# Optimization experiments

Hardware: AMD Instinct MI355X
Metric: run time of the kernel (lower is better)

The kernel has to match this reference:

```python
import jax, jax.numpy as jnp
import numpy as np

D_MODEL, NHEAD, INT_DIM = 1024, 16, 4096
HEAD_DIM = D_MODEL // NHEAD
EPS = 1e-5


def _layernorm(x, gamma, beta):
    mu = jnp.mean(x, axis=-1, keepdims=True)
    var = jnp.var(x, axis=-1, keepdims=True)
    return (x - mu) * jax.lax.rsqrt(var + EPS) * gamma + beta


def setup_inputs() -> dict:
    key = jax.random.key(0)
    ks = jax.random.split(key, 16)
    B, T = 2, 2048
    s = 0.02
    inp = {
        'x': jax.random.normal(ks[0], (B, T, D_MODEL), dtype=jnp.float32),
        'Wq': jax.random.normal(ks[1], (D_MODEL, D_MODEL), dtype=jnp.float32) * s,
        'bq': jnp.zeros((D_MODEL,), jnp.float32),
        'Wk': jax.random.normal(ks[2], (D_MODEL, D_MODEL), dtype=jnp.float32) * s,
        'bk': jnp.zeros((D_MODEL,), jnp.float32),
        'Wv': jax.random.normal(ks[3], (D_MODEL, D_MODEL), dtype=jnp.float32) * s,
        'bv': jnp.zeros((D_MODEL,), jnp.float32),
        'Wo': jax.random.normal(ks[4], (D_MODEL, D_MODEL), dtype=jnp.float32) * s,
        'bo': jnp.zeros((D_MODEL,), jnp.float32),
        'ln1_g': jnp.ones((D_MODEL,), jnp.float32),
        'ln1_b': jnp.zeros((D_MODEL,), jnp.float32),
        'ln2_g': jnp.ones((D_MODEL,), jnp.float32),
        'ln2_b': jnp.zeros((D_MODEL,), jnp.float32),
        'W1': jax.random.normal(ks[5], (D_MODEL, INT_DIM), dtype=jnp.float32) * s,
        'b1': jnp.zeros((INT_DIM,), jnp.float32),
        'W2': jax.random.normal(ks[6], (INT_DIM, D_MODEL), dtype=jnp.float32) * s,
        'b2': jnp.zeros((D_MODEL,), jnp.float32),
    }
    return inp


def reference(x, Wq, bq, Wk, bk, Wv, bv, Wo, bo, ln1_g, ln1_b, ln2_g, ln2_b, W1, b1, W2, b2):
    B, T, D = x.shape
    # projections
    q = (x @ Wq + bq).reshape(B, T, NHEAD, HEAD_DIM).transpose(0, 2, 1, 3)
    k = (x @ Wk + bk).reshape(B, T, NHEAD, HEAD_DIM).transpose(0, 2, 1, 3)
    v = (x @ Wv + bv).reshape(B, T, NHEAD, HEAD_DIM).transpose(0, 2, 1, 3)
    # attention: [B,H,T,T] scores, softmax over keys
    scores = jnp.einsum('bhqd,bhkd->bhqk', q, k) / jnp.sqrt(jnp.float32(HEAD_DIM))
    attn = jax.nn.softmax(scores, axis=-1)
    out = jnp.einsum('bhqk,bhkd->bhqd', attn, v)
    out = out.transpose(0, 2, 1, 3).reshape(B, T, D)
    attn_output = out @ Wo + bo
    # residual + layernorm 1
    h = _layernorm(x + attn_output, ln1_g, ln1_b)
    # FFN
    ff = jax.nn.relu(h @ W1 + b1) @ W2 + b2
    # residual + layernorm 2
    return _layernorm(h + ff, ln2_g, ln2_b)
```

## Files before the change

kernel.cpp:

```cpp
#include <hip/hip_runtime.h>
#include <cstdint>

#define DEVI __device__ __forceinline__

typedef float f32x4 __attribute__((ext_vector_type(4)));
typedef __bf16 bf16x8 __attribute__((ext_vector_type(8)));
typedef unsigned short u16;
typedef unsigned int u32;
typedef unsigned long long u64;

DEVI u16 bf16bits(float f) {
    u32 u = __builtin_bit_cast(u32, f);
    u32 r = u + 0x7fffu + ((u >> 16) & 1u);
    return (u16)(r >> 16);
}

DEVI u32 pack2bf(float a, float b) {
    u16 x = __builtin_bit_cast(u16, (__bf16)a);
    u16 y = __builtin_bit_cast(u16, (__bf16)b);
    return (u32)x | ((u32)y << 16);
}

DEVI void gload16(const void* g, const void* l) {
    __builtin_amdgcn_global_load_lds(
        (const __attribute__((address_space(1))) void*)(u64)(uintptr_t)g,
        (__attribute__((address_space(3))) void*)(u32)(uintptr_t)l,
        16, 0, 0);
}

__global__ __launch_bounds__(256) void cast_bf16_kernel(const float* __restrict__ in,
                                                        u16* __restrict__ out, int n4) {
    int i = blockIdx.x * 256 + threadIdx.x;
    if (i < n4) {
        float4 v = ((const float4*)in)[i];
        u32 lo = bf16bits(v.x) | ((u32)bf16bits(v.y) << 16);
        u32 hi = bf16bits(v.z) | ((u32)bf16bits(v.w) << 16);
        ((uint2*)out)[i] = make_uint2(lo, hi);
    }
}

DEVI void tpose_body(const float* __restrict__ src, u16* __restrict__ dst, int K_, int N_) {
    __shared__ float t[64][65];
    int k0 = blockIdx.x * 64, n0 = blockIdx.y * 64;
    int tid = threadIdx.x;
#pragma unroll
    for (int i = 0; i < 16; i++) {
        int idx = i * 256 + tid;
        int r = idx >> 6, c = idx & 63;
        t[r][c] = src[(u64)(k0 + r) * N_ + n0 + c];
    }
    __syncthreads();
#pragma unroll
    for (int i = 0; i < 16; i++) {
        int idx = i * 256 + tid;
        int r = idx >> 6, c = idx & 63;
        dst[(u64)(n0 + r) * K_ + k0 + c] = bf16bits(t[c][r]);
    }
}

__global__ __launch_bounds__(256) void transpose_cast_kernel(const float* __restrict__ src,
                                                             u16* __restrict__ dst,
                                                             int K_, int N_) {
    tpose_body(src, dst, K_, N_);
}

__global__ __launch_bounds__(256) void transpose_cast4_kernel(
    const float* __restrict__ s0, const float* __restrict__ s1,
    const float* __restrict__ s2, const float* __restrict__ s3,
    u16* __restrict__ d0, u16* __restrict__ d1, u16* __restrict__ d2, u16* __restrict__ d3) {
    int z = blockIdx.z;
    const float* src = z == 0 ? s0 : z == 1 ? s1 : z == 2 ? s2 : s3;
    u16* dst = z == 0 ? d0 : z == 1 ? d1 : z == 2 ? d2 : d3;
    tpose_body(src, dst, 1024, 1024);
}

enum { MODE_QK = 0, MODE_VT = 1, MODE_RESID = 2, MODE_RELU = 3 };

DEVI void gemm_core(const u16* __restrict__ A, const u16* __restrict__ Bt, int K_,
                    u16* ldsA, u16* ldsB, f32x4 (&acc)[4][4], int m0, int n0) {
    const int tid = threadIdx.x;
    const int lane = tid & 63;
    const int wid = tid >> 6;
    const int wr = wid >> 1, wc = wid & 1;
    const int l15 = lane & 15, l4 = lane >> 4;

    for (int kt = 0; kt < K_; kt += 64) {
        __syncthreads();
#pragma unroll
        for (int i = 0; i < 4; i++) {
            int s = i * 256 + tid;
            int row = s >> 3, c = s & 7;
            gload16(A + (u64)(m0 + row) * K_ + kt + ((c ^ (row & 7)) * 8),
                    (const char*)ldsA + s * 16);
        }
#pragma unroll
        for (int i = 0; i < 4; i++) {
            int s = i * 256 + tid;
            int row = s >> 3, c = s & 7;
            gload16(Bt + (u64)(n0 + row) * K_ + kt + ((c ^ (row & 7)) * 8),
                    (const char*)ldsB + s * 16);
        }
        __syncthreads();
#pragma unroll
        for (int ks = 0; ks < 2; ks++) {
            bf16x8 af[4], bfr[4];
#pragma unroll
            for (int mi = 0; mi < 4; mi++) {
                int row = wr * 64 + mi * 16 + l15;
                af[mi] = *(const bf16x8*)((const char*)ldsA + row * 128 +
                                          (((ks * 4 + l4) ^ (row & 7)) * 16));
            }
#pragma unroll
            for (int ni = 0; ni < 4; ni++) {
                int row = wc * 64 + ni * 16 + l15;
                bfr[ni] = *(const bf16x8*)((const char*)ldsB + row * 128 +
                                           (((ks * 4 + l4) ^ (row & 7)) * 16));
            }
            __builtin_amdgcn_s_setprio(1);
#pragma unroll
            for (int mi = 0; mi < 4; mi++)
#pragma unroll
                for (int ni = 0; ni < 4; ni++)
                    acc[mi][ni] = __builtin_amdgcn_mfma_f32_16x16x32_bf16(
                        af[mi], bfr[ni], acc[mi][ni], 0, 0, 0);
            __builtin_amdgcn_s_setprio(0);
        }
    }
}

template <int MODE>
DEVI void gemm_epilogue(f32x4 (&acc)[4][4], const float* __restrict__ bias,
                        const float* __restrict__ resid, void* __restrict__ outp,
                        int N_, int m0, int n0) {
    const int tid = threadIdx.x;
    const int lane = tid & 63;
    const int wid = tid >> 6;
    const int wr = wid >> 1, wc = wid & 1;
    const int l15 = lane & 15, l4 = lane >> 4;
#pragma unroll
    for (int mi = 0; mi < 4; mi++) {
#pragma unroll
        for (int ni = 0; ni < 4; ni++) {
            const int n = n0 + wc * 64 + ni * 16 + l15;
            const float bv = bias[n];
            const int mb = m0 + wr * 64 + mi * 16 + l4 * 4;
            if (MODE == MODE_VT) {
                const int b = mb >> 11, t = mb & 2047;
                const int hh = n >> 6, d = n & 63;
                u32 lo = pack2bf(acc[mi][ni][0] + bv, acc[mi][ni][1] + bv);
                u32 hi = pack2bf(acc[mi][ni][2] + bv, acc[mi][ni][3] + bv);
                u64 idx = ((u64)((b << 4) + hh) * 64 + d) * 2048 + t;
                *(uint2*)((u16*)outp + idx) = make_uint2(lo, hi);
            } else {
#pragma unroll
                for (int r = 0; r < 4; r++) {
                    const int m = mb + r;
                    const float v = acc[mi][ni][r] + bv;
                    if (MODE == MODE_QK) {
                        const int b = m >> 11, t = m & 2047;
                        const int hh = n >> 6, d = n & 63;
                        ((u16*)outp)[(((u64)((b << 4) + hh) * 2048 + t) << 6) + d] = bf16bits(v);
                    } else if (MODE == MODE_RESID) {
                        const u64 i2 = (u64)m * N_ + n;
                        ((float*)outp)[i2] = v + resid[i2];
                    } else {
                        ((u16*)outp)[(u64)m * N_ + n] = bf16bits(fmaxf(v, 0.f));
                    }
                }
            }
        }
    }
}

template <int MODE>
__global__ __launch_bounds__(256, 2)
void gemm_kernel(const u16* __restrict__ A, const u16* __restrict__ Bt,
                 const float* __restrict__ bias, const float* __restrict__ resid,
                 void* __restrict__ outp, int N_, int K_) {
    __shared__ u16 ldsA[128 * 64];
    __shared__ u16 ldsB[128 * 64];
    const int m0 = blockIdx.x * 128;
    const int n0 = blockIdx.y * 128;
    f32x4 acc[4][4];
#pragma unroll
    for (int i = 0; i < 4; i++)
#pragma unroll
        for (int j = 0; j < 4; j++) acc[i][j] = (f32x4){0.f, 0.f, 0.f, 0.f};
    gemm_core(A, Bt, K_, ldsA, ldsB, acc, m0, n0);
    gemm_epilogue<MODE>(acc, bias, resid, outp, N_, m0, n0);
}

__global__ __launch_bounds__(256, 2)
void gemm_qkv_kernel(const u16* __restrict__ A,
                     const u16* __restrict__ Wq, const u16* __restrict__ Wk,
                     const u16* __restrict__ Wv,
                     const float* __restrict__ bq, const float* __restrict__ bk,
                     const float* __restrict__ bv,
                     u16* __restrict__ Qo, u16* __restrict__ Ko, u16* __restrict__ Vo) {
    __shared__ u16 ldsA[128 * 64];
    __shared__ u16 ldsB[128 * 64];
    const int z = blockIdx.z;
    const u16* Bt = z == 0 ? Wq : z == 1 ? Wk : Wv;
    const float* bias = z == 0 ? bq : z == 1 ? bk : bv;
    const int m0 = blockIdx.x * 128;
    const int n0 = blockIdx.y * 128;
    f32x4 acc[4][4];
#pragma unroll
    for (int i = 0; i < 4; i++)
#pragma unroll
        for (int j = 0; j < 4; j++) acc[i][j] = (f32x4){0.f, 0.f, 0.f, 0.f};
    gemm_core(A, Bt, 1024, ldsA, ldsB, acc, m0, n0);
    if (z == 2)
        gemm_epilogue<MODE_VT>(acc, bias, nullptr, Vo, 1024, m0, n0);
    else
        gemm_epilogue<MODE_QK>(acc, bias, nullptr, z == 0 ? Qo : Ko, 1024, m0, n0);
}

#define LOG2E 1.44269504088896f

__global__ __launch_bounds__(256, 4)
void attn_kernel(const u16* __restrict__ Qg, const u16* __restrict__ Kg,
                 const u16* __restrict__ Vtg, u16* __restrict__ Og) {
    __shared__ u16 ldsK[2][64 * 64];
    __shared__ u16 ldsV[2][64 * 64];
    __shared__ u16 ldsP[4][16 * 64];
    const int tid = threadIdx.x;
    const int lane = tid & 63;
    const int w = tid >> 6;
    const int l15 = lane & 15, l4 = lane >> 4;
    const int id = blockIdx.x;
    const int swz = (id & 7) * 128 + (id >> 3);
    const int bh = swz >> 5;
    const int qblk = swz & 31;
    const u64 kvbase = (u64)bh * 2048 * 64;
    const int qw0 = qblk * 64 + w * 16;

    auto stage = [&](int buf, int kt) {
#pragma unroll
        for (int i = 0; i < 2; i++) {
            int s = i * 256 + tid; int row = s >> 3, c = s & 7;
            gload16(Kg + kvbase + (u64)(kt + row) * 64 + ((c ^ (row & 7)) * 8),
                    (const char*)ldsK[buf] + s * 16);
        }
#pragma unroll
        for (int i = 0; i < 2; i++) {
            int s = i * 256 + tid; int row = s >> 3, c = s & 7;
            gload16(Vtg + kvbase + (u64)row * 2048 + kt + ((c ^ (row & 7)) * 8),
                    (const char*)ldsV[buf] + s * 16);
        }
    };

    stage(0, 0);

    bf16x8 aq[2];
#pragma unroll
    for (int ks = 0; ks < 2; ks++)
        aq[ks] = *(const bf16x8*)(Qg + kvbase + (u64)(qw0 + l15) * 64 + ks * 32 + l4 * 8);

    f32x4 acco[4];
#pragma unroll
    for (int i = 0; i < 4; i++) acco[i] = (f32x4){0.f, 0.f, 0.f, 0.f};
    float lacc = 0.f;

    u16* ldsPw = ldsP[w];
    const float sc = 0.125f * LOG2E;

    asm volatile("s_waitcnt vmcnt(0)" ::: "memory");
    __builtin_amdgcn_s_barrier();

    for (int t = 0; t < 32; t++) {
        const int cur = t & 1;
        if (t < 31) stage(cur ^ 1, (t + 1) * 64);
        const u16* K_ = ldsK[cur];
        const u16* V_ = ldsV[cur];

        f32x4 sf[4];
#pragma unroll
        for (int f = 0; f < 4; f++) sf[f] = (f32x4){0.f, 0.f, 0.f, 0.f};
#pragma unroll
        for (int ks = 0; ks < 2; ks++) {
            bf16x8 ak[4];
#pragma unroll
            for (int f = 0; f < 4; f++) {
                int row = f * 16 + l15;
                ak[f] = *(const bf16x8*)((const char*)K_ + row * 128 +
                                         (((ks * 4 + l4) ^ (row & 7)) * 16));
            }
            __builtin_amdgcn_s_setprio(1);
#pragma unroll
            for (int f = 0; f < 4; f++)
                sf[f] = __builtin_amdgcn_mfma_f32_16x16x32_bf16(ak[f], aq[ks], sf[f], 0, 0, 0);
            __builtin_amdgcn_s_setprio(0);
        }

#pragma unroll
        for (int f = 0; f < 4; f++) {
            float p0 = exp2f(sf[f][0] * sc);
            float p1 = exp2f(sf[f][1] * sc);
            float p2 = exp2f(sf[f][2] * sc);
            float p3 = exp2f(sf[f][3] * sc);
            lacc += (p0 + p1) + (p2 + p3);
            *(uint2*)((char*)ldsPw + l15 * 128 +
                      (((f * 2 + (l4 >> 1)) ^ (l15 & 7)) * 16) + (l4 & 1) * 8) =
                make_uint2(pack2bf(p0, p1), pack2bf(p2, p3));
        }

#pragma unroll
        for (int ks = 0; ks < 2; ks++) {
            bf16x8 pfrag = *(const bf16x8*)((const char*)ldsPw + l15 * 128 +
                                            (((ks * 4 + l4) ^ (l15 & 7)) * 16));
#pragma unroll
            for (int nf = 0; nf < 4; nf++) {
                int row = nf * 16 + l15;
                bf16x8 av = *(const bf16x8*)((const char*)V_ + row * 128 +
                                             (((ks * 4 + l4) ^ (row & 7)) * 16));
                __builtin_amdgcn_s_setprio(1);
                acco[nf] = __builtin_amdgcn_mfma_f32_16x16x32_bf16(av, pfrag, acco[nf], 0, 0, 0);
                __builtin_amdgcn_s_setprio(0);
            }
        }

        asm volatile("s_waitcnt vmcnt(0)" ::: "memory");
        __builtin_amdgcn_s_barrier();
    }

    lacc += __shfl_xor(lacc, 16, 64);
    lacc += __shfl_xor(lacc, 32, 64);
    const float inv = 1.f / lacc;

    const int b = bh >> 4, h = bh & 15;
    const int tq = qw0 + l15;
#pragma unroll
    for (int nf = 0; nf < 4; nf++) {
        const int d = nf * 16 + l4 * 4;
        u32 lo = pack2bf(acco[nf][0] * inv, acco[nf][1] * inv);
        u32 hi = pack2bf(acco[nf][2] * inv, acco[nf][3] * inv);
        *(uint2*)(Og + ((u64)(b * 2048 + tq) << 10) + h * 64 + d) = make_uint2(lo, hi);
    }
}

template <bool WB16>
__global__ __launch_bounds__(256, 4)
void ln_kernel(const float* __restrict__ in, const float* __restrict__ gam,
               const float* __restrict__ bet, float* __restrict__ outf,
               u16* __restrict__ outb) {
    __shared__ float red[2][4];
    const int row = blockIdx.x;
    const int tid = threadIdx.x;
    float4 v = ((const float4*)(in + (u64)row * 1024))[tid];
    float s = v.x + v.y + v.z + v.w;
    float sq = v.x * v.x + v.y * v.y + v.z * v.z + v.w * v.w;
#pragma unroll
    for (int sh = 1; sh < 64; sh <<= 1) {
        s += __shfl_xor(s, sh, 64);
        sq += __shfl_xor(sq, sh, 64);
    }
    if ((tid & 63) == 0) { red[0][tid >> 6] = s; red[1][tid >> 6] = sq; }
    __syncthreads();
    s = red[0][0] + red[0][1] + red[0][2] + red[0][3];
    sq = red[1][0] + red[1][1] + red[1][2] + red[1][3];
    float mu = s * (1.f / 1024.f);
    float var = sq * (1.f / 1024.f) - mu * mu;
    float inv = rsqrtf(var + 1e-5f);
    float4 g = ((const float4*)gam)[tid];
    float4 bb = ((const float4*)bet)[tid];
    float4 o;
    o.x = (v.x - mu) * inv * g.x + bb.x;
    o.y = (v.y - mu) * inv * g.y + bb.y;
    o.z = (v.z - mu) * inv * g.z + bb.z;
    o.w = (v.w - mu) * inv * g.w + bb.w;
    ((float4*)(outf + (u64)row * 1024))[tid] = o;
    if (WB16) {
        u32 lo = pack2bf(o.x, o.y);
        u32 hi = pack2bf(o.z, o.w);
        ((uint2*)(outb + (u64)row * 1024))[tid] = make_uint2(lo, hi);
    }
}

extern "C" void kernel_launch(void* const* d_in, const int* in_sizes, int n_in,
                              void* d_out, int out_size, void* d_ws, size_t ws_size,
                              hipStream_t stream) {
    (void)in_sizes; (void)n_in; (void)out_size; (void)ws_size;
    const float* x  = (const float*)d_in[0];
    const float* Wq = (const float*)d_in[1];
    const float* bq = (const float*)d_in[2];
    const float* Wk = (const float*)d_in[3];
    const float* bk = (const float*)d_in[4];
    const float* Wv = (const float*)d_in[5];
    const float* bv = (const float*)d_in[6];
    const float* Wo = (const float*)d_in[7];
    const float* bo = (const float*)d_in[8];
    const float* g1 = (const float*)d_in[9];
    const float* be1 = (const float*)d_in[10];
    const float* g2 = (const float*)d_in[11];
    const float* be2 = (const float*)d_in[12];
    const float* W1 = (const float*)d_in[13];
    const float* b1 = (const float*)d_in[14];
    const float* W2 = (const float*)d_in[15];
    const float* b2 = (const float*)d_in[16];

    char* ws = (char*)d_ws;
    const u64 MB = 1024ull * 1024ull;
    u16* xb    = (u16*)(ws + 0);
    u16* Wqt   = (u16*)(ws + 8 * MB);
    u16* Wkt   = (u16*)(ws + 10 * MB);
    u16* Wvt   = (u16*)(ws + 12 * MB);
    u16* Wot   = (u16*)(ws + 14 * MB);
    u16* W1t   = (u16*)(ws + 16 * MB);
    u16* W2t   = (u16*)(ws + 24 * MB);
    u16* Qb    = (u16*)(ws + 32 * MB);
    u16* Kb    = (u16*)(ws + 40 * MB);
    u16* Vtb   = (u16*)(ws + 48 * MB);
    u16* Ob    = (u16*)(ws + 56 * MB);
    float* pre1 = (float*)(ws + 64 * MB);
    float* hf  = (float*)(ws + 80 * MB);
    u16* hb    = (u16*)(ws + 96 * MB);
    u16* ffb   = (u16*)(ws + 104 * MB);
    float* pre2 = (float*)(ws + 64 * MB);

    cast_bf16_kernel<<<4096, 256, 0, stream>>>(x, xb, 1024 * 1024);
    transpose_cast4_kernel<<<dim3(16, 16, 4), 256, 0, stream>>>(Wq, Wk, Wv, Wo,
                                                                Wqt, Wkt, Wvt, Wot);
    transpose_cast_kernel<<<dim3(16, 64), 256, 0, stream>>>(W1, W1t, 1024, 4096);
    transpose_cast_kernel<<<dim3(64, 16), 256, 0, stream>>>(W2, W2t, 4096, 1024);

    gemm_qkv_kernel<<<dim3(32, 8, 3), 256, 0, stream>>>(xb, Wqt, Wkt, Wvt,
                                                        bq, bk, bv, Qb, Kb, Vtb);

    attn_kernel<<<1024, 256, 0, stream>>>(Qb, Kb, Vtb, Ob);

    gemm_kernel<MODE_RESID><<<dim3(32, 8), 256, 0, stream>>>(Ob, Wot, bo, x, pre1, 1024, 1024);
    ln_kernel<true><<<4096, 256, 0, stream>>>(pre1, g1, be1, hf, hb);
    gemm_kernel<MODE_RELU><<<dim3(32, 32), 256, 0, stream>>>(hb, W1t, b1, nullptr, ffb, 4096, 1024);
    gemm_kernel<MODE_RESID><<<dim3(32, 8), 256, 0, stream>>>(ffb, W2t, b2, hf, pre2, 1024, 4096);
    ln_kernel<false><<<4096, 256, 0, stream>>>(pre2, g2, be2, (float*)d_out, nullptr);
}
```

Baseline: 252.0 us.

## Rewrite attention with 32x32 MFMA, register-resident P via permlane swap, folded Q scale

The attention kernel moves from 16x16x32 to 32x32x16 bf16 MFMA, with 2 waves per block each owning 32 query rows. The softmax probabilities now stay in registers and are rearranged with v_permlane32_swap into the B-operand layout, which removes the LDS round trip for P. The 1/sqrt(d)*log2e scale is folded into the Q projection epilogue so the inner exp2 loop drops a multiply. Risks are higher register pressure, fewer threads per block to stage K/V tiles, and lower occupancy from launch_bounds(128,2).

```diff
diff --git a/kernel.cpp b/kernel.cpp
--- a/kernel.cpp
+++ b/kernel.cpp
@@ -4,10 +4,15 @@
 #define DEVI __device__ __forceinline__
 
 typedef float f32x4 __attribute__((ext_vector_type(4)));
+typedef float f32x16 __attribute__((ext_vector_type(16)));
 typedef __bf16 bf16x8 __attribute__((ext_vector_type(8)));
+typedef unsigned int u32x4v __attribute__((ext_vector_type(4)));
 typedef unsigned short u16;
 typedef unsigned int u32;
 typedef unsigned long long u64;
+
+#define LOG2E 1.44269504088896f
+#define QSCALE (0.125f * LOG2E)
 
 DEVI u16 bf16bits(float f) {
     u32 u = __builtin_bit_cast(u32, f);
@@ -131,7 +136,7 @@
 template <int MODE>
 DEVI void gemm_epilogue(f32x4 (&acc)[4][4], const float* __restrict__ bias,
                         const float* __restrict__ resid, void* __restrict__ outp,
-                        int N_, int m0, int n0) {
+                        int N_, int m0, int n0, float scale) {
     const int tid = threadIdx.x;
     const int lane = tid & 63;
     const int wid = tid >> 6;
@@ -159,7 +164,8 @@
                     if (MODE == MODE_QK) {
                         const int b = m >> 11, t = m & 2047;
                         const int hh = n >> 6, d = n & 63;
-                        ((u16*)outp)[(((u64)((b << 4) + hh) * 2048 + t) << 6) + d] = bf16bits(v);
+                        ((u16*)outp)[(((u64)((b << 4) + hh) * 2048 + t) << 6) + d] =
+                            bf16bits(v * scale);
                     } else if (MODE == MODE_RESID) {
                         const u64 i2 = (u64)m * N_ + n;
                         ((float*)outp)[i2] = v + resid[i2];
@@ -187,7 +193,7 @@
 #pragma unroll
         for (int j = 0; j < 4; j++) acc[i][j] = (f32x4){0.f, 0.f, 0.f, 0.f};
     gemm_core(A, Bt, K_, ldsA, ldsB, acc, m0, n0);
-    gemm_epilogue<MODE>(acc, bias, resid, outp, N_, m0, n0);
+    gemm_epilogue<MODE>(acc, bias, resid, outp, N_, m0, n0, 1.f);
 }
 
 __global__ __launch_bounds__(256, 2)
@@ -211,40 +217,38 @@
         for (int j = 0; j < 4; j++) acc[i][j] = (f32x4){0.f, 0.f, 0.f, 0.f};
     gemm_core(A, Bt, 1024, ldsA, ldsB, acc, m0, n0);
     if (z == 2)
-        gemm_epilogue<MODE_VT>(acc, bias, nullptr, Vo, 1024, m0, n0);
+        gemm_epilogue<MODE_VT>(acc, bias, nullptr, Vo, 1024, m0, n0, 1.f);
     else
-        gemm_epilogue<MODE_QK>(acc, bias, nullptr, z == 0 ? Qo : Ko, 1024, m0, n0);
-}
-
-#define LOG2E 1.44269504088896f
-
-__global__ __launch_bounds__(256, 4)
+        gemm_epilogue<MODE_QK>(acc, bias, nullptr, z == 0 ? Qo : Ko, 1024, m0, n0,
+                               z == 0 ? QSCALE : 1.f);
+}
+
+__global__ __launch_bounds__(128, 2)
 void attn_kernel(const u16* __restrict__ Qg, const u16* __restrict__ Kg,
                  const u16* __restrict__ Vtg, u16* __restrict__ Og) {
     __shared__ u16 ldsK[2][64 * 64];
     __shared__ u16 ldsV[2][64 * 64];
-    __shared__ u16 ldsP[4][16 * 64];
     const int tid = threadIdx.x;
     const int lane = tid & 63;
     const int w = tid >> 6;
-    const int l15 = lane & 15, l4 = lane >> 4;
+    const int l31 = lane & 31, l5 = lane >> 5;
     const int id = blockIdx.x;
     const int swz = (id & 7) * 128 + (id >> 3);
     const int bh = swz >> 5;
     const int qblk = swz & 31;
     const u64 kvbase = (u64)bh * 2048 * 64;
-    const int qw0 = qblk * 64 + w * 16;
+    const int qw0 = qblk * 64 + w * 32;
 
     auto stage = [&](int buf, int kt) {
 #pragma unroll
-        for (int i = 0; i < 2; i++) {
-            int s = i * 256 + tid; int row = s >> 3, c = s & 7;
+        for (int i = 0; i < 4; i++) {
+            int s = i * 128 + tid; int row = s >> 3, c = s & 7;
             gload16(Kg + kvbase + (u64)(kt + row) * 64 + ((c ^ (row & 7)) * 8),
                     (const char*)ldsK[buf] + s * 16);
         }
 #pragma unroll
-        for (int i = 0; i < 2; i++) {
-            int s = i * 256 + tid; int row = s >> 3, c = s & 7;
+        for (int i = 0; i < 4; i++) {
+            int s = i * 128 + tid; int row = s >> 3, c = s & 7;
             gload16(Vtg + kvbase + (u64)row * 2048 + kt + ((c ^ (row & 7)) * 8),
                     (const char*)ldsV[buf] + s * 16);
         }
@@ -252,18 +256,14 @@
 
     stage(0, 0);
 
-    bf16x8 aq[2];
-#pragma unroll
-    for (int ks = 0; ks < 2; ks++)
-        aq[ks] = *(const bf16x8*)(Qg + kvbase + (u64)(qw0 + l15) * 64 + ks * 32 + l4 * 8);
-
-    f32x4 acco[4];
-#pragma unroll
-    for (int i = 0; i < 4; i++) acco[i] = (f32x4){0.f, 0.f, 0.f, 0.f};
-    float lacc = 0.f;
-
-    u16* ldsPw = ldsP[w];
-    const float sc = 0.125f * LOG2E;
+    bf16x8 aq[4];
+#pragma unroll
+    for (int dc = 0; dc < 4; dc++)
+        aq[dc] = *(const bf16x8*)(Qg + kvbase + (u64)(qw0 + l31) * 64 + dc * 16 + l5 * 8);
+
+    f32x16 acco[2] = {};
+    float la0 = 0.f, la1 = 0.f, la2 = 0.f, la3 = 0.f;
+    const f32x16 fz = {};
 
     asm volatile("s_waitcnt vmcnt(0)" ::: "memory");
     __builtin_amdgcn_s_barrier();
@@ -274,48 +274,56 @@
         const u16* K_ = ldsK[cur];
         const u16* V_ = ldsV[cur];
 
-        f32x4 sf[4];
-#pragma unroll
-        for (int f = 0; f < 4; f++) sf[f] = (f32x4){0.f, 0.f, 0.f, 0.f};
-#pragma unroll
-        for (int ks = 0; ks < 2; ks++) {
+        f32x16 sf[2];
+#pragma unroll
+        for (int f = 0; f < 2; f++) {
+            const int row = f * 32 + l31;
             bf16x8 ak[4];
 #pragma unroll
-            for (int f = 0; f < 4; f++) {
-                int row = f * 16 + l15;
-                ak[f] = *(const bf16x8*)((const char*)K_ + row * 128 +
-                                         (((ks * 4 + l4) ^ (row & 7)) * 16));
+            for (int dc = 0; dc < 4; dc++)
+                ak[dc] = *(const bf16x8*)((const char*)K_ + row * 128 +
+                                          (((dc * 2 + l5) ^ (row & 7)) * 16));
+            __builtin_amdgcn_s_setprio(1);
+            sf[f] = __builtin_amdgcn_mfma_f32_32x32x16_bf16(ak[0], aq[0], fz, 0, 0, 0);
+#pragma unroll
+            for (int dc = 1; dc < 4; dc++)
+                sf[f] = __builtin_amdgcn_mfma_f32_32x32x16_bf16(ak[dc], aq[dc], sf[f], 0, 0, 0);
+            __builtin_amdgcn_s_setprio(0);
+        }
+
+#pragma unroll
+        for (int f = 0; f < 2; f++) {
+#pragma unroll
+            for (int k = 0; k < 16; k += 4) {
+                float p0 = exp2f(sf[f][k + 0]);
+                float p1 = exp2f(sf[f][k + 1]);
+                float p2 = exp2f(sf[f][k + 2]);
+                float p3 = exp2f(sf[f][k + 3]);
+                sf[f][k + 0] = p0; sf[f][k + 1] = p1;
+                sf[f][k + 2] = p2; sf[f][k + 3] = p3;
+                la0 += p0; la1 += p1; la2 += p2; la3 += p3;
             }
-            __builtin_amdgcn_s_setprio(1);
-#pragma unroll
-            for (int f = 0; f < 4; f++)
-                sf[f] = __builtin_amdgcn_mfma_f32_16x16x32_bf16(ak[f], aq[ks], sf[f], 0, 0, 0);
-            __builtin_amdgcn_s_setprio(0);
-        }
-
-#pragma unroll
-        for (int f = 0; f < 4; f++) {
-            float p0 = exp2f(sf[f][0] * sc);
-            float p1 = exp2f(sf[f][1] * sc);
-            float p2 = exp2f(sf[f][2] * sc);
-            float p3 = exp2f(sf[f][3] * sc);
-            lacc += (p0 + p1) + (p2 + p3);
-            *(uint2*)((char*)ldsPw + l15 * 128 +
-                      (((f * 2 + (l4 >> 1)) ^ (l15 & 7)) * 16) + (l4 & 1) * 8) =
-                make_uint2(pack2bf(p0, p1), pack2bf(p2, p3));
-        }
-
-#pragma unroll
-        for (int ks = 0; ks < 2; ks++) {
-            bf16x8 pfrag = *(const bf16x8*)((const char*)ldsPw + l15 * 128 +
-                                            (((ks * 4 + l4) ^ (l15 & 7)) * 16));
-#pragma unroll
-            for (int nf = 0; nf < 4; nf++) {
-                int row = nf * 16 + l15;
+        }
+
+#pragma unroll
+        for (int c = 0; c < 4; c++) {
+            const int F = c >> 1;
+            const int rb = 8 * (c & 1);
+            u32 w0 = pack2bf(sf[F][rb + 0], sf[F][rb + 1]);
+            u32 w1 = pack2bf(sf[F][rb + 2], sf[F][rb + 3]);
+            u32 w2 = pack2bf(sf[F][rb + 4], sf[F][rb + 5]);
+            u32 w3 = pack2bf(sf[F][rb + 6], sf[F][rb + 7]);
+            asm volatile("v_permlane32_swap_b32 %0, %1" : "+v"(w0), "+v"(w2));
+            asm volatile("v_permlane32_swap_b32 %0, %1" : "+v"(w1), "+v"(w3));
+            u32x4v pw = {w0, w1, w2, w3};
+            bf16x8 pb = __builtin_bit_cast(bf16x8, pw);
+#pragma unroll
+            for (int db = 0; db < 2; db++) {
+                const int row = db * 32 + l31;
                 bf16x8 av = *(const bf16x8*)((const char*)V_ + row * 128 +
-                                             (((ks * 4 + l4) ^ (row & 7)) * 16));
+                                             (((c * 2 + l5) ^ (row & 7)) * 16));
                 __builtin_amdgcn_s_setprio(1);
-                acco[nf] = __builtin_amdgcn_mfma_f32_16x16x32_bf16(av, pfrag, acco[nf], 0, 0, 0);
+                acco[db] = __builtin_amdgcn_mfma_f32_32x32x16_bf16(av, pb, acco[db], 0, 0, 0);
                 __builtin_amdgcn_s_setprio(0);
             }
         }
@@ -324,19 +332,21 @@
         __builtin_amdgcn_s_barrier();
     }
 
-    lacc += __shfl_xor(lacc, 16, 64);
+    float lacc = (la0 + la1) + (la2 + la3);
     lacc += __shfl_xor(lacc, 32, 64);
     const float inv = 1.f / lacc;
 
     const int b = bh >> 4, h = bh & 15;
-    const int tq = qw0 + l15;
-#pragma unroll
-    for (int nf = 0; nf < 4; nf++) {
-        const int d = nf * 16 + l4 * 4;
-        u32 lo = pack2bf(acco[nf][0] * inv, acco[nf][1] * inv);
-        u32 hi = pack2bf(acco[nf][2] * inv, acco[nf][3] * inv);
-        *(uint2*)(Og + ((u64)(b * 2048 + tq) << 10) + h * 64 + d) = make_uint2(lo, hi);
-    }
+    const int tq = qw0 + l31;
+#pragma unroll
+    for (int db = 0; db < 2; db++)
+#pragma unroll
+        for (int rq = 0; rq < 4; rq++) {
+            const int d = 32 * db + 8 * rq + 4 * l5;
+            u32 lo = pack2bf(acco[db][4 * rq + 0] * inv, acco[db][4 * rq + 1] * inv);
+            u32 hi = pack2bf(acco[db][4 * rq + 2] * inv, acco[db][4 * rq + 3] * inv);
+            *(uint2*)(Og + ((u64)(b * 2048 + tq) << 10) + h * 64 + d) = make_uint2(lo, hi);
+        }
 }
 
 template <bool WB16>
@@ -427,7 +437,7 @@
     gemm_qkv_kernel<<<dim3(32, 8, 3), 256, 0, stream>>>(xb, Wqt, Wkt, Wvt,
                                                         bq, bk, bv, Qb, Kb, Vtb);
 
-    attn_kernel<<<1024, 256, 0, stream>>>(Qb, Kb, Vtb, Ob);
+    attn_kernel<<<1024, 128, 0, stream>>>(Qb, Kb, Vtb, Ob);
 
     gemm_kernel<MODE_RESID><<<dim3(32, 8), 256, 0, stream>>>(Ob, Wot, bo, x, pre1, 1024, 1024);
     ln_kernel<true><<<4096, 256, 0, stream>>>(pre1, g1, be1, hf, hb);
```

Measured after the change: 259.7 us. 1.03x slower.

## Fold softmax scale into Q projection and shuffle P in registers via permlane swaps

Applied to the files above, without the earlier changes.

The softmax scale (1/sqrt(d)·log2e) is now applied to Q in the QKV GEMM epilogue, so the attention loop drops a multiply per score. The P tile is no longer written to and read back from per-wave LDS. Lanes exchange the packed bf16 probabilities with v_permlane32/16_swap so they arrive in MFMA B-operand layout. The V fragment loads are batched ahead of the MFMAs, and launch bounds rise to 5 blocks per CU since LDS use drops. This relies on the permlane lane mapping matching the fragment layout, and Q rounded to bf16 after scaling changes numerics slightly.

```diff
diff --git a/kernel.cpp b/kernel.cpp
--- a/kernel.cpp
+++ b/kernel.cpp
@@ -5,9 +5,13 @@
 
 typedef float f32x4 __attribute__((ext_vector_type(4)));
 typedef __bf16 bf16x8 __attribute__((ext_vector_type(8)));
+typedef unsigned int u32x4v __attribute__((ext_vector_type(4)));
 typedef unsigned short u16;
 typedef unsigned int u32;
 typedef unsigned long long u64;
+
+#define LOG2E 1.44269504088896f
+#define QSCALE (0.125f * LOG2E)
 
 DEVI u16 bf16bits(float f) {
     u32 u = __builtin_bit_cast(u32, f);
@@ -131,7 +135,7 @@
 template <int MODE>
 DEVI void gemm_epilogue(f32x4 (&acc)[4][4], const float* __restrict__ bias,
                         const float* __restrict__ resid, void* __restrict__ outp,
-                        int N_, int m0, int n0) {
+                        int N_, int m0, int n0, float scale) {
     const int tid = threadIdx.x;
     const int lane = tid & 63;
     const int wid = tid >> 6;
@@ -159,7 +163,8 @@
                     if (MODE == MODE_QK) {
                         const int b = m >> 11, t = m & 2047;
                         const int hh = n >> 6, d = n & 63;
-                        ((u16*)outp)[(((u64)((b << 4) + hh) * 2048 + t) << 6) + d] = bf16bits(v);
+                        ((u16*)outp)[(((u64)((b << 4) + hh) * 2048 + t) << 6) + d] =
+                            bf16bits(v * scale);
                     } else if (MODE == MODE_RESID) {
                         const u64 i2 = (u64)m * N_ + n;
                         ((float*)outp)[i2] = v + resid[i2];
@@ -187,7 +192,7 @@
 #pragma unroll
         for (int j = 0; j < 4; j++) acc[i][j] = (f32x4){0.f, 0.f, 0.f, 0.f};
     gemm_core(A, Bt, K_, ldsA, ldsB, acc, m0, n0);
-    gemm_epilogue<MODE>(acc, bias, resid, outp, N_, m0, n0);
+    gemm_epilogue<MODE>(acc, bias, resid, outp, N_, m0, n0, 1.f);
 }
 
 __global__ __launch_bounds__(256, 2)
@@ -211,19 +216,17 @@
         for (int j = 0; j < 4; j++) acc[i][j] = (f32x4){0.f, 0.f, 0.f, 0.f};
     gemm_core(A, Bt, 1024, ldsA, ldsB, acc, m0, n0);
     if (z == 2)
-        gemm_epilogue<MODE_VT>(acc, bias, nullptr, Vo, 1024, m0, n0);
+        gemm_epilogue<MODE_VT>(acc, bias, nullptr, Vo, 1024, m0, n0, 1.f);
     else
-        gemm_epilogue<MODE_QK>(acc, bias, nullptr, z == 0 ? Qo : Ko, 1024, m0, n0);
-}
-
-#define LOG2E 1.44269504088896f
-
-__global__ __launch_bounds__(256, 4)
+        gemm_epilogue<MODE_QK>(acc, bias, nullptr, z == 0 ? Qo : Ko, 1024, m0, n0,
+                               z == 0 ? QSCALE : 1.f);
+}
+
+__global__ __launch_bounds__(256, 5)
 void attn_kernel(const u16* __restrict__ Qg, const u16* __restrict__ Kg,
                  const u16* __restrict__ Vtg, u16* __restrict__ Og) {
     __shared__ u16 ldsK[2][64 * 64];
     __shared__ u16 ldsV[2][64 * 64];
-    __shared__ u16 ldsP[4][16 * 64];
     const int tid = threadIdx.x;
     const int lane = tid & 63;
     const int w = tid >> 6;
@@ -260,10 +263,7 @@
     f32x4 acco[4];
 #pragma unroll
     for (int i = 0; i < 4; i++) acco[i] = (f32x4){0.f, 0.f, 0.f, 0.f};
-    float lacc = 0.f;
-
-    u16* ldsPw = ldsP[w];
-    const float sc = 0.125f * LOG2E;
+    float la0 = 0.f, la1 = 0.f;
 
     asm volatile("s_waitcnt vmcnt(0)" ::: "memory");
     __builtin_amdgcn_s_barrier();
@@ -293,37 +293,50 @@
             __builtin_amdgcn_s_setprio(0);
         }
 
+        u32 A[4], B[4];
 #pragma unroll
         for (int f = 0; f < 4; f++) {
-            float p0 = exp2f(sf[f][0] * sc);
-            float p1 = exp2f(sf[f][1] * sc);
-            float p2 = exp2f(sf[f][2] * sc);
-            float p3 = exp2f(sf[f][3] * sc);
-            lacc += (p0 + p1) + (p2 + p3);
-            *(uint2*)((char*)ldsPw + l15 * 128 +
-                      (((f * 2 + (l4 >> 1)) ^ (l15 & 7)) * 16) + (l4 & 1) * 8) =
-                make_uint2(pack2bf(p0, p1), pack2bf(p2, p3));
-        }
+            float p0 = exp2f(sf[f][0]);
+            float p1 = exp2f(sf[f][1]);
+            float p2 = exp2f(sf[f][2]);
+            float p3 = exp2f(sf[f][3]);
+            la0 += p0 + p2;
+            la1 += p1 + p3;
+            A[f] = pack2bf(p0, p1);
+            B[f] = pack2bf(p2, p3);
+        }
+        asm volatile("v_permlane32_swap_b32 %0, %1" : "+v"(A[0]), "+v"(A[1]));
+        asm volatile("v_permlane16_swap_b32 %0, %1" : "+v"(A[0]), "+v"(A[1]));
+        asm volatile("v_permlane32_swap_b32 %0, %1" : "+v"(B[0]), "+v"(B[1]));
+        asm volatile("v_permlane16_swap_b32 %0, %1" : "+v"(B[0]), "+v"(B[1]));
+        asm volatile("v_permlane32_swap_b32 %0, %1" : "+v"(A[2]), "+v"(A[3]));
+        asm volatile("v_permlane16_swap_b32 %0, %1" : "+v"(A[2]), "+v"(A[3]));
+        asm volatile("v_permlane32_swap_b32 %0, %1" : "+v"(B[2]), "+v"(B[3]));
+        asm volatile("v_permlane16_swap_b32 %0, %1" : "+v"(B[2]), "+v"(B[3]));
 
 #pragma unroll
         for (int ks = 0; ks < 2; ks++) {
-            bf16x8 pfrag = *(const bf16x8*)((const char*)ldsPw + l15 * 128 +
-                                            (((ks * 4 + l4) ^ (l15 & 7)) * 16));
+            u32x4v pw = {A[2 * ks], B[2 * ks], A[2 * ks + 1], B[2 * ks + 1]};
+            bf16x8 pfrag = __builtin_bit_cast(bf16x8, pw);
+            bf16x8 av[4];
 #pragma unroll
             for (int nf = 0; nf < 4; nf++) {
                 int row = nf * 16 + l15;
-                bf16x8 av = *(const bf16x8*)((const char*)V_ + row * 128 +
-                                             (((ks * 4 + l4) ^ (row & 7)) * 16));
-                __builtin_amdgcn_s_setprio(1);
-                acco[nf] = __builtin_amdgcn_mfma_f32_16x16x32_bf16(av, pfrag, acco[nf], 0, 0, 0);
-                __builtin_amdgcn_s_setprio(0);
+                av[nf] = *(const bf16x8*)((const char*)V_ + row * 128 +
+                                          (((ks * 4 + l4) ^ (row & 7)) * 16));
             }
+            __builtin_amdgcn_s_setprio(1);
+#pragma unroll
+            for (int nf = 0; nf < 4; nf++)
+                acco[nf] = __builtin_amdgcn_mfma_f32_16x16x32_bf16(av[nf], pfrag, acco[nf], 0, 0, 0);
+            __builtin_amdgcn_s_setprio(0);
         }
 
         asm volatile("s_waitcnt vmcnt(0)" ::: "memory");
         __builtin_amdgcn_s_barrier();
     }
 
+    float lacc = la0 + la1;
     lacc += __shfl_xor(lacc, 16, 64);
     lacc += __shfl_xor(lacc, 32, 64);
     const float inv = 1.f / lacc;
```

After: 248.5 us. Within noise of the previous version (-1.4%).
